# Kernel tuning notes

Hardware: AMD Instinct MI355X
Metric: run time of the kernel (lower is better)

## Reference

```python
import jax, jax.numpy as jnp
import numpy as np

N, L2, C = 4096, 49, 128   # lmax=6 -> (lmax+1)**2 = 49
RES = 18                   # grid resolution (beta, alpha)


def setup_inputs() -> dict:
    key = jax.random.key(0)
    k1, k2, k3 = jax.random.split(key, 3)
    inputs = jax.random.normal(k1, (N, L2, C), dtype=jnp.float32)
    # Stand-ins for the precomputed spherical-harmonic transform matrices
    # (to_grid_mat / from_grid_mat), shape (res_beta, res_alpha, (lmax+1)**2).
    W_to = jax.random.normal(k2, (RES, RES, L2), dtype=jnp.float32) / jnp.sqrt(jnp.float32(L2))
    W_from = jax.random.normal(k3, (RES, RES, L2), dtype=jnp.float32) / jnp.sqrt(jnp.float32(RES * RES))
    return {"inputs": inputs, "W_to": W_to, "W_from": W_from}


def reference(inputs, W_to, W_from):
    # to_grid: coefficients -> real-space S2 grid  (n, beta, alpha, c)
    grid = jnp.einsum('bai,nic->nbac', W_to, inputs)
    # elementwise self tensor product on the grid
    grid = grid * grid
    # from_grid: project back to spherical-harmonic coefficients (n, i, c)
    outputs = jnp.einsum('bai,nbac->nic', W_from, grid)
    return outputs
```

## Files before the change

### kernel.cpp

```cpp
#include <hip/hip_runtime.h>


#define NN    4096
#define L2D   49
#define CCH   128
#define GTOT  324
#define MT1P  22
#define KC2   11

typedef __attribute__((ext_vector_type(8))) short bf16x8;
typedef __attribute__((ext_vector_type(4))) float f32x4;

#define WT_SHORTS (MT1P * 2 * 64 * 8)
#define WF_SHORTS (4 * KC2 * 64 * 8)

__device__ __forceinline__ short f2bf(float f) {
    union { float f; unsigned u; } x; x.f = f;
    return (short)((x.u + 0x7fffu + ((x.u >> 16) & 1u)) >> 16);
}

__device__ __forceinline__ unsigned cvtpk(float lo, float hi) {
    unsigned r;
    asm("v_cvt_pk_bf16_f32 %0, %1, %2" : "=v"(r) : "v"(lo), "v"(hi));
    return r;
}

__global__ void prep_w_kernel(const float* __restrict__ Wt,
                              const float* __restrict__ Wf,
                              short* __restrict__ WtF,
                              short* __restrict__ WfF)
{
    int idx = blockIdx.x * 256 + threadIdx.x;
    if (idx < WT_SHORTS) {
        int j = idx & 7, lane = (idx >> 3) & 63, kcx = (idx >> 9) & 1, mt = idx >> 10;
        int g = mt * 16 + (lane & 15);
        int i = kcx * 32 + (lane >> 4) * 8 + j;
        WtF[idx] = f2bf((g < GTOT && i < L2D) ? Wt[g * L2D + i] : 0.0f);
    } else if (idx < WT_SHORTS + WF_SHORTS) {
        int e = idx - WT_SHORTS;
        int j = e & 7, lane = (e >> 3) & 63, t = e >> 9;
        int kc2 = t % KC2, it = t / KC2;
        int i = it * 16 + (lane & 15);
        int g = kc2 * 32 + (j >> 2) * 16 + (lane >> 4) * 4 + (j & 3);
        WfF[e] = f2bf((g < GTOT && i < L2D) ? Wf[g * L2D + i] : 0.0f);
    }
}

__global__ __launch_bounds__(256, 4)
void stp_mfma6_kernel(const float* __restrict__ inp,
                      const short* __restrict__ WtF,
                      const short* __restrict__ WfF,
                      float* __restrict__ out)
{
    const int tid  = threadIdx.x;
    const int lane = tid & 63;
    const int wave = tid >> 6;
    const int lm   = lane & 15;
    const int quad = lane >> 4;

    const int task = blockIdx.x * 4 + wave;
    const int n    = task >> 2;
    const int q    = task & 3;

    const float* __restrict__ Xn = inp + (size_t)n * (L2D * CCH);

    bf16x8 Bx[2][2];
    #pragma unroll
    for (int t = 0; t < 2; ++t) {
        const int c = q * 32 + t * 16 + lm;
        #pragma unroll
        for (int kcx = 0; kcx < 2; ++kcx) {
            union { bf16x8 v; unsigned u[4]; } b;
            #pragma unroll
            for (int p = 0; p < 4; ++p) {
                const int i0 = kcx * 32 + quad * 8 + 2 * p;
                float v0 = (i0     < L2D) ? Xn[(i0    ) * CCH + c] : 0.0f;
                float v1 = (i0 + 1 < L2D) ? Xn[(i0 + 1) * CCH + c] : 0.0f;
                b.u[p] = cvtpk(v0, v1);
            }
            Bx[t][kcx] = b.v;
        }
    }

    f32x4 acc2[4][2];
    #pragma unroll
    for (int it = 0; it < 4; ++it)
        #pragma unroll
        for (int t = 0; t < 2; ++t)
            acc2[it][t] = (f32x4){0.0f, 0.0f, 0.0f, 0.0f};

    #pragma unroll 1
    for (int kc2 = 0; kc2 < KC2; ++kc2) {
        bf16x8 Wtf[2][2];
        #pragma unroll
        for (int tt = 0; tt < 2; ++tt)
            #pragma unroll
            for (int kcx = 0; kcx < 2; ++kcx)
                Wtf[tt][kcx] = *(const bf16x8*)&WtF[(((2 * kc2 + tt) * 2 + kcx) * 64 + lane) * 8];
        bf16x8 Wff[4];
        #pragma unroll
        for (int it = 0; it < 4; ++it)
            Wff[it] = *(const bf16x8*)&WfF[((it * KC2 + kc2) * 64 + lane) * 8];

        #pragma unroll
        for (int t = 0; t < 2; ++t) {
            union { bf16x8 v; unsigned u[4]; } bg;
            #pragma unroll
            for (int tt = 0; tt < 2; ++tt) {
                f32x4 g = (f32x4){0.0f, 0.0f, 0.0f, 0.0f};
                g = __builtin_amdgcn_mfma_f32_16x16x32_bf16(Wtf[tt][0], Bx[t][0], g, 0, 0, 0);
                g = __builtin_amdgcn_mfma_f32_16x16x32_bf16(Wtf[tt][1], Bx[t][1], g, 0, 0, 0);
                bg.u[tt * 2 + 0] = cvtpk(g[0] * g[0], g[1] * g[1]);
                bg.u[tt * 2 + 1] = cvtpk(g[2] * g[2], g[3] * g[3]);
            }
            #pragma unroll
            for (int it = 0; it < 4; ++it)
                acc2[it][t] = __builtin_amdgcn_mfma_f32_16x16x32_bf16(Wff[it], bg.v, acc2[it][t], 0, 0, 0);
        }
    }

    float* __restrict__ On = out + (size_t)n * (L2D * CCH);
    #pragma unroll
    for (int it = 0; it < 4; ++it) {
        #pragma unroll
        for (int t = 0; t < 2; ++t) {
            const int c = q * 32 + t * 16 + lm;
            #pragma unroll
            for (int r = 0; r < 4; ++r) {
                const int i = it * 16 + quad * 4 + r;
                if (i < L2D) On[i * CCH + c] = acc2[it][t][r];
            }
        }
    }
}

extern "C" void kernel_launch(void* const* d_in, const int* in_sizes, int n_in,
                              void* d_out, int out_size, void* d_ws, size_t ws_size,
                              hipStream_t stream) {
    const float* inp = (const float*)d_in[0];
    const float* Wt  = (const float*)d_in[1];
    const float* Wf  = (const float*)d_in[2];
    float* out = (float*)d_out;

    short* WtF = (short*)d_ws;
    short* WfF = WtF + WT_SHORTS;

    const int prep_threads = WT_SHORTS + WF_SHORTS;
    prep_w_kernel<<<(prep_threads + 255) / 256, 256, 0, stream>>>(Wt, Wf, WtF, WfF);
    stp_mfma6_kernel<<<4096, 256, 0, stream>>>(inp, WtF, WfF, out);
}
```

Baseline: 231.2 us.

## Switch to 32x32x16 MFMA tiles with 64 channels per wave

Replaces the 16x16x32 bf16 MFMA chain with 32x32x16 MFMAs, rearranging the packed weight layouts so the grid-chunk output of the first matmul feeds straight into the second as a B operand. Each wave now handles 64 channels of one sample instead of 32, halving the grid and cutting per-element weight-fragment loads. The intent is to get more throughput from the larger MFMA shape and reuse each weight fragment across more columns. The cost is more accumulator registers (f32x16), which lowers the occupancy target to 3 blocks per CU, and extra padding waste since 49 rows are padded to 64.

```diff
diff --git a/kernel.cpp b/kernel.cpp
--- a/kernel.cpp
+++ b/kernel.cpp
@@ -5,14 +5,13 @@
 #define L2D   49
 #define CCH   128
 #define GTOT  324
-#define MT1P  22
 #define KC2   11
 
-typedef __attribute__((ext_vector_type(8))) short bf16x8;
-typedef __attribute__((ext_vector_type(4))) float f32x4;
+typedef __attribute__((ext_vector_type(8)))  short bf16x8;
+typedef __attribute__((ext_vector_type(16))) float f32x16;
 
-#define WT_SHORTS (MT1P * 2 * 64 * 8)
-#define WF_SHORTS (4 * KC2 * 64 * 8)
+#define WT_SHORTS (KC2 * 4 * 64 * 8)
+#define WF_SHORTS (2 * KC2 * 2 * 64 * 8)
 
 __device__ __forceinline__ short f2bf(float f) {
     union { float f; unsigned u; } x; x.f = f;
@@ -32,22 +31,26 @@
 {
     int idx = blockIdx.x * 256 + threadIdx.x;
     if (idx < WT_SHORTS) {
-        int j = idx & 7, lane = (idx >> 3) & 63, kcx = (idx >> 9) & 1, mt = idx >> 10;
-        int g = mt * 16 + (lane & 15);
-        int i = kcx * 32 + (lane >> 4) * 8 + j;
+        int j = idx & 7, lane = (idx >> 3) & 63, ki = (idx >> 9) & 3, kc2 = idx >> 11;
+        int m = lane & 31, H = lane >> 5;
+        int gwc = ((m >> 3) & 1) * 16 + ((m >> 2) & 1) * 8 + (m >> 4) * 4 + (m & 3);
+        int g = kc2 * 32 + gwc;
+        int i = ki * 16 + H * 8 + j;
         WtF[idx] = f2bf((g < GTOT && i < L2D) ? Wt[g * L2D + i] : 0.0f);
     } else if (idx < WT_SHORTS + WF_SHORTS) {
         int e = idx - WT_SHORTS;
-        int j = e & 7, lane = (e >> 3) & 63, t = e >> 9;
-        int kc2 = t % KC2, it = t / KC2;
-        int i = it * 16 + (lane & 15);
-        int g = kc2 * 32 + (j >> 2) * 16 + (lane >> 4) * 4 + (j & 3);
+        int j = e & 7, lane = (e >> 3) & 63, cc = (e >> 9) & 1;
+        int u = e >> 10;
+        int kc2 = u % KC2, it = u / KC2;
+        int m = lane & 31, H = lane >> 5;
+        int i = it * 32 + m;
+        int g = kc2 * 32 + cc * 16 + H * 8 + j;
         WfF[e] = f2bf((g < GTOT && i < L2D) ? Wf[g * L2D + i] : 0.0f);
     }
 }
 
-__global__ __launch_bounds__(256, 4)
-void stp_mfma6_kernel(const float* __restrict__ inp,
+__global__ __launch_bounds__(256, 3)
+void stp_mfma7_kernel(const float* __restrict__ inp,
                       const short* __restrict__ WtF,
                       const short* __restrict__ WfF,
                       float* __restrict__ out)
@@ -55,80 +58,88 @@
     const int tid  = threadIdx.x;
     const int lane = tid & 63;
     const int wave = tid >> 6;
-    const int lm   = lane & 15;
-    const int quad = lane >> 4;
+    const int m    = lane & 31;
+    const int H    = lane >> 5;
 
     const int task = blockIdx.x * 4 + wave;
-    const int n    = task >> 2;
-    const int q    = task & 3;
+    const int n    = task >> 1;
+    const int h    = task & 1;
 
     const float* __restrict__ Xn = inp + (size_t)n * (L2D * CCH);
 
-    bf16x8 Bx[2][2];
+    bf16x8 Bx[2][4];
     #pragma unroll
-    for (int t = 0; t < 2; ++t) {
-        const int c = q * 32 + t * 16 + lm;
+    for (int cq = 0; cq < 2; ++cq) {
+        const int c = h * 64 + cq * 32 + m;
         #pragma unroll
-        for (int kcx = 0; kcx < 2; ++kcx) {
+        for (int ki = 0; ki < 4; ++ki) {
             union { bf16x8 v; unsigned u[4]; } b;
             #pragma unroll
             for (int p = 0; p < 4; ++p) {
-                const int i0 = kcx * 32 + quad * 8 + 2 * p;
+                const int i0 = ki * 16 + H * 8 + 2 * p;
                 float v0 = (i0     < L2D) ? Xn[(i0    ) * CCH + c] : 0.0f;
                 float v1 = (i0 + 1 < L2D) ? Xn[(i0 + 1) * CCH + c] : 0.0f;
                 b.u[p] = cvtpk(v0, v1);
             }
-            Bx[t][kcx] = b.v;
+            Bx[cq][ki] = b.v;
         }
     }
 
-    f32x4 acc2[4][2];
+    f32x16 acc2[2][2];
     #pragma unroll
-    for (int it = 0; it < 4; ++it)
+    for (int it = 0; it < 2; ++it)
         #pragma unroll
-        for (int t = 0; t < 2; ++t)
-            acc2[it][t] = (f32x4){0.0f, 0.0f, 0.0f, 0.0f};
+        for (int cq = 0; cq < 2; ++cq)
+            acc2[it][cq] = (f32x16)(0.0f);
 
     #pragma unroll 1
     for (int kc2 = 0; kc2 < KC2; ++kc2) {
-        bf16x8 Wtf[2][2];
+        bf16x8 Wtf[4];
         #pragma unroll
-        for (int tt = 0; tt < 2; ++tt)
+        for (int ki = 0; ki < 4; ++ki)
+            Wtf[ki] = *(const bf16x8*)&WtF[((kc2 * 4 + ki) * 64 + lane) * 8];
+        bf16x8 Wff[2][2];
+        #pragma unroll
+        for (int it = 0; it < 2; ++it)
             #pragma unroll
-            for (int kcx = 0; kcx < 2; ++kcx)
-                Wtf[tt][kcx] = *(const bf16x8*)&WtF[(((2 * kc2 + tt) * 2 + kcx) * 64 + lane) * 8];
-        bf16x8 Wff[4];
-        #pragma unroll
-        for (int it = 0; it < 4; ++it)
-            Wff[it] = *(const bf16x8*)&WfF[((it * KC2 + kc2) * 64 + lane) * 8];
+            for (int cc = 0; cc < 2; ++cc)
+                Wff[it][cc] = *(const bf16x8*)&WfF[(((it * KC2 + kc2) * 2 + cc) * 64 + lane) * 8];
 
         #pragma unroll
-        for (int t = 0; t < 2; ++t) {
-            union { bf16x8 v; unsigned u[4]; } bg;
+        for (int cq = 0; cq < 2; ++cq) {
+            f32x16 g = (f32x16)(0.0f);
             #pragma unroll
-            for (int tt = 0; tt < 2; ++tt) {
-                f32x4 g = (f32x4){0.0f, 0.0f, 0.0f, 0.0f};
-                g = __builtin_amdgcn_mfma_f32_16x16x32_bf16(Wtf[tt][0], Bx[t][0], g, 0, 0, 0);
-                g = __builtin_amdgcn_mfma_f32_16x16x32_bf16(Wtf[tt][1], Bx[t][1], g, 0, 0, 0);
-                bg.u[tt * 2 + 0] = cvtpk(g[0] * g[0], g[1] * g[1]);
-                bg.u[tt * 2 + 1] = cvtpk(g[2] * g[2], g[3] * g[3]);
+            for (int ki = 0; ki < 4; ++ki)
+                g = __builtin_amdgcn_mfma_f32_32x32x16_bf16(Wtf[ki], Bx[cq][ki], g, 0, 0, 0);
+
+            union { bf16x8 v; unsigned u[4]; } bg0, bg1;
+            bg0.u[0] = cvtpk(g[0] * g[0],   g[1] * g[1]);
+            bg0.u[1] = cvtpk(g[2] * g[2],   g[3] * g[3]);
+            bg0.u[2] = cvtpk(g[8] * g[8],   g[9] * g[9]);
+            bg0.u[3] = cvtpk(g[10] * g[10], g[11] * g[11]);
+            bg1.u[0] = cvtpk(g[4] * g[4],   g[5] * g[5]);
+            bg1.u[1] = cvtpk(g[6] * g[6],   g[7] * g[7]);
+            bg1.u[2] = cvtpk(g[12] * g[12], g[13] * g[13]);
+            bg1.u[3] = cvtpk(g[14] * g[14], g[15] * g[15]);
+
+            #pragma unroll
+            for (int it = 0; it < 2; ++it) {
+                acc2[it][cq] = __builtin_amdgcn_mfma_f32_32x32x16_bf16(Wff[it][0], bg0.v, acc2[it][cq], 0, 0, 0);
+                acc2[it][cq] = __builtin_amdgcn_mfma_f32_32x32x16_bf16(Wff[it][1], bg1.v, acc2[it][cq], 0, 0, 0);
             }
-            #pragma unroll
-            for (int it = 0; it < 4; ++it)
-                acc2[it][t] = __builtin_amdgcn_mfma_f32_16x16x32_bf16(Wff[it], bg.v, acc2[it][t], 0, 0, 0);
         }
     }
 
     float* __restrict__ On = out + (size_t)n * (L2D * CCH);
     #pragma unroll
-    for (int it = 0; it < 4; ++it) {
+    for (int it = 0; it < 2; ++it) {
         #pragma unroll
-        for (int t = 0; t < 2; ++t) {
-            const int c = q * 32 + t * 16 + lm;
+        for (int cq = 0; cq < 2; ++cq) {
+            const int c = h * 64 + cq * 32 + m;
             #pragma unroll
-            for (int r = 0; r < 4; ++r) {
-                const int i = it * 16 + quad * 4 + r;
-                if (i < L2D) On[i * CCH + c] = acc2[it][t][r];
+            for (int r = 0; r < 16; ++r) {
+                const int i = it * 32 + (r & 3) + 8 * (r >> 2) + 4 * H;
+                if (i < L2D) On[i * CCH + c] = acc2[it][cq][r];
             }
         }
     }
@@ -147,5 +158,5 @@
 
     const int prep_threads = WT_SHORTS + WF_SHORTS;
     prep_w_kernel<<<(prep_threads + 255) / 256, 256, 0, stream>>>(Wt, Wf, WtF, WfF);
-    stp_mfma6_kernel<<<4096, 256, 0, stream>>>(inp, WtF, WfF, out);
+    stp_mfma7_kernel<<<2048, 256, 0, stream>>>(inp, WtF, WfF, out);
 }
```

Measured after the change: 210.6 us. -8.9%, faster.
